# Performance work log

Hardware: AMD Instinct MI355X
Metric: run time of the kernel (lower is better)

The kernel has to match this reference:

```python
import jax, jax.numpy as jnp
import numpy as np


def _ln(x, g, b, eps=1e-5):
    m = x.mean(-1, keepdims=True)
    v = x.var(-1, keepdims=True)
    return (x - m) / jnp.sqrt(v + eps) * g + b


def setup_inputs() -> dict:
    key = jax.random.key(0)
    ks = jax.random.split(key, 10)
    N, H, E, OUT, L = 4096, 256, 131072, 64, 6
    s = 1.0 / np.sqrt(H)
    return {
        "x": jax.random.normal(ks[0], (N, H), jnp.float32),
        "edge_index": jax.random.randint(ks[1], (2, E), 0, N, jnp.int32),
        "sage_wl": jax.random.normal(ks[2], (L, H, H), jnp.float32) * s,   # lin_l (neighbors, has bias)
        "sage_wr": jax.random.normal(ks[3], (L, H, H), jnp.float32) * s,   # lin_r (root, no bias)
        "sage_bl": jnp.zeros((L, H), jnp.float32),
        "ln_g": jnp.ones((L - 1, H), jnp.float32),
        "ln_b": jnp.zeros((L - 1, H), jnp.float32),
        "conv_w": jax.random.normal(ks[4], (3, H, H, 3), jnp.float32) * (1.0 / np.sqrt(3 * H)),  # [layer,O,I,K]
        "conv_b": jnp.zeros((3, H), jnp.float32),
        "cnorm_g": jnp.ones((3, H), jnp.float32),
        "cnorm_b": jnp.zeros((3, H), jnp.float32),
        "in_proj_w": jax.random.normal(ks[5], (6 * H, 2 * H), jnp.float32) * (1.0 / np.sqrt(2 * H)),
        "in_proj_b": jnp.zeros((6 * H,), jnp.float32),
        "out_proj_w": jax.random.normal(ks[6], (2 * H, 2 * H), jnp.float32) * (1.0 / np.sqrt(2 * H)),
        "out_proj_b": jnp.zeros((2 * H,), jnp.float32),
        "anorm_g": jnp.ones((2 * H,), jnp.float32),
        "anorm_b": jnp.zeros((2 * H,), jnp.float32),
        "fuse_w": jax.random.normal(ks[7], (OUT, 2 * H), jnp.float32) * (1.0 / np.sqrt(2 * H)),
        "fuse_b": jnp.zeros((OUT,), jnp.float32),
    }


def reference(x, edge_index, sage_wl, sage_wr, sage_bl, ln_g, ln_b,
              conv_w, conv_b, cnorm_g, cnorm_b,
              in_proj_w, in_proj_b, out_proj_w, out_proj_b,
              anorm_g, anorm_b, fuse_w, fuse_b):
    # Dropout layers act as identity (eval mode).
    N, H = x.shape
    L = sage_wl.shape[0]
    src, dst = edge_index[0], edge_index[1]
    deg = jax.ops.segment_sum(jnp.ones(src.shape[0], x.dtype), dst, num_segments=N)
    deg = jnp.maximum(deg, 1.0)[:, None]
    h = x
    for i in range(L):
        res = h
        # SAGEConv: mean-aggregate neighbor features (gather/scatter), then two linears
        agg = jax.ops.segment_sum(h[src], dst, num_segments=N) / deg
        h = agg @ sage_wl[i].T + sage_bl[i] + h @ sage_wr[i].T
        if i < L - 1:
            h = _ln(h, ln_g[i], ln_b[i])
        h = jax.nn.relu(h) + res  # residual (shapes always match: in==hidden)
    gnn_out = h                                   # [N, H]

    # CNN branch over the node axis: [1, H, N]
    c = gnn_out.T[None]
    for j in range(3):
        c = jax.lax.conv_general_dilated(c, conv_w[j], (1,), ((1, 1),),
                                         dimension_numbers=("NCH", "OIH", "NCH"))
        c = jax.nn.relu(c + conv_b[j][None, :, None])
        c = _ln(c.transpose(0, 2, 1), cnorm_g[j], cnorm_b[j]).transpose(0, 2, 1)
    cnn_out = c[0].T                              # [N, H]

    fused = jnp.concatenate([gnn_out, cnn_out], axis=1)  # [N, 2H]
    E2 = fused.shape[1]
    heads = 4
    hd = E2 // heads
    qkv = fused @ in_proj_w.T + in_proj_b
    q, k, v = jnp.split(qkv, 3, axis=1)
    split_heads = lambda t: t.reshape(N, heads, hd).transpose(1, 0, 2)  # [h, N, hd]
    q, k, v = split_heads(q), split_heads(k), split_heads(v)
    scores = jnp.einsum("hnd,hmd->hnm", q, k) / np.sqrt(hd).astype(np.float32)
    a = jax.nn.softmax(scores, axis=-1)
    o = jnp.einsum("hnm,hmd->hnd", a, v).transpose(1, 0, 2).reshape(N, E2)
    o = o @ out_proj_w.T + out_proj_b
    o = _ln(o, anorm_g, anorm_b)
    return o @ fuse_w.T + fuse_b                  # [N, out_channels]
```

## Files before the change

kernel.cpp:

```cpp
#include <hip/hip_runtime.h>

#define NN 4096
#define HH 256
#define EE 131072

__device__ __constant__ float LN_EPS = 1e-5f;
#define ATT_SCALE 0.08838834764831845f
#define ATT_SHIFT 30.0f

typedef __attribute__((ext_vector_type(8))) short bf16x8_t;
typedef __attribute__((ext_vector_type(4))) float f32x4_t;

__device__ inline ushort f2b(float f) {
  uint u = __float_as_uint(f);
  uint r = (u + 0x7FFF + ((u >> 16) & 1)) >> 16;
  return (ushort)r;
}

__global__ void hist_kernel(const int* __restrict__ ei, int* __restrict__ cnt) {
  int e = blockIdx.x * blockDim.x + threadIdx.x;
  if (e < EE) atomicAdd(&cnt[ei[EE + e]], 1);
}

__global__ __launch_bounds__(1024) void scan_kernel(int* __restrict__ cnt_cursor,
                                                    int* __restrict__ rowptr,
                                                    float* __restrict__ invdeg) {
  __shared__ int part[1024];
  int t = threadIdx.x;
  int base = t * 4;
  int cs[4];
  int s = 0;
  for (int u = 0; u < 4; ++u) { cs[u] = cnt_cursor[base + u]; s += cs[u]; }
  part[t] = s;
  __syncthreads();
  for (int off = 1; off < 1024; off <<= 1) {
    int add = (t >= off) ? part[t - off] : 0;
    int v = part[t];
    __syncthreads();
    part[t] = v + add;
    __syncthreads();
  }
  int excl = (t > 0) ? part[t - 1] : 0;
  for (int u = 0; u < 4; ++u) {
    rowptr[base + u] = excl;
    cnt_cursor[base + u] = excl;
    invdeg[base + u] = 1.0f / (float)max(cs[u], 1);
    excl += cs[u];
  }
  if (t == 1023) rowptr[NN] = excl;
}

__global__ void fill_kernel(const int* __restrict__ ei, int* __restrict__ cursor,
                            int* __restrict__ col) {
  int e = blockIdx.x * blockDim.x + threadIdx.x;
  if (e < EE) {
    int d = ei[EE + e];
    int p = atomicAdd(&cursor[d], 1);
    col[p] = ei[e];
  }
}

__global__ __launch_bounds__(256) void castw(const float* __restrict__ in,
                                             ushort* __restrict__ out) {
  int i4 = (blockIdx.x * 256 + threadIdx.x) * 4;
  float4 v = *(const float4*)(in + i4);
  ushort4 w;
  w.x = f2b(v.x); w.y = f2b(v.y); w.z = f2b(v.z); w.w = f2b(v.w);
  *(ushort4*)(out + i4) = w;
}

__global__ __launch_bounds__(256) void castconv(const float* __restrict__ w,
                                                ushort* __restrict__ o) {
  int idx = blockIdx.x * 256 + threadIdx.x;
  int j = idx / 196608;
  int rem = idx - j * 196608;
  int oc = rem / 768;
  int kk = rem - oc * 768;
  int ks = kk >> 8, ii = kk & 255;
  o[idx] = f2b(w[j * 196608 + oc * 768 + ii * 3 + ks]);
}

__global__ __launch_bounds__(64) void agg_kernel(const float* __restrict__ h,
                                                 const int* __restrict__ rowptr,
                                                 const int* __restrict__ col,
                                                 const float* __restrict__ invdeg,
                                                 ushort* __restrict__ aggb) {
  int n = blockIdx.x;
  int t = threadIdx.x;
  int s = rowptr[n], e = rowptr[n + 1];
  float4 acc = make_float4(0.f, 0.f, 0.f, 0.f);
  for (int j = s; j < e; ++j) {
    int c = col[j];
    const float4 v = *(const float4*)(h + (size_t)c * HH + t * 4);
    acc.x += v.x; acc.y += v.y; acc.z += v.z; acc.w += v.w;
  }
  float id = invdeg[n];
  ushort4 w;
  w.x = f2b(acc.x * id); w.y = f2b(acc.y * id);
  w.z = f2b(acc.z * id); w.w = f2b(acc.w * id);
  *(ushort4*)(aggb + (size_t)n * HH + t * 4) = w;
}

__global__ __launch_bounds__(256) void gemm_mfma(
    const ushort* __restrict__ A0, const ushort* __restrict__ A1,
    const ushort* __restrict__ B0, const ushort* __restrict__ B1,
    const float* __restrict__ bias, float* __restrict__ Cf, ushort* __restrict__ Cb,
    int M, int Nn, int K, int KHA, int KHB, int relu) {
  __shared__ ushort Alds[64][40];
  __shared__ ushort Blds[128][40];
  int t = threadIdx.x;
  int w = t >> 6, l = t & 63, quad = l >> 4, lr = l & 15;
  int wm = w & 1, wn = w >> 1;
  int m0 = blockIdx.x * 64, n0 = blockIdx.y * 128;
  int sr = t >> 2, sc8 = (t & 3) * 8;
  f32x4_t acc[2][4];
#pragma unroll
  for (int s = 0; s < 2; ++s)
#pragma unroll
    for (int q = 0; q < 4; ++q) acc[s][q] = (f32x4_t){0.f, 0.f, 0.f, 0.f};

  for (int k0 = 0; k0 < K; k0 += 32) {
    int kk = k0 + sc8;
    const ushort* ap = (kk < KHA) ? (A0 + (size_t)(m0 + sr) * KHA + kk)
                                  : (A1 + (size_t)(m0 + sr) * (K - KHA) + (kk - KHA));
    uint4 av = *(const uint4*)ap;
    const ushort* bp0 = (kk < KHB) ? (B0 + (size_t)(n0 + sr) * KHB + kk)
                                   : (B1 + (size_t)(n0 + sr) * (K - KHB) + (kk - KHB));
    uint4 bv0 = *(const uint4*)bp0;
    const ushort* bp1 = (kk < KHB) ? (B0 + (size_t)(n0 + 64 + sr) * KHB + kk)
                                   : (B1 + (size_t)(n0 + 64 + sr) * (K - KHB) + (kk - KHB));
    uint4 bv1 = *(const uint4*)bp1;
    __syncthreads();
    *(uint4*)&Alds[sr][sc8] = av;
    *(uint4*)&Blds[sr][sc8] = bv0;
    *(uint4*)&Blds[64 + sr][sc8] = bv1;
    __syncthreads();
    bf16x8_t af[2], bf[4];
#pragma unroll
    for (int s = 0; s < 2; ++s)
      af[s] = *(const bf16x8_t*)&Alds[wm * 32 + s * 16 + lr][quad * 8];
#pragma unroll
    for (int q = 0; q < 4; ++q)
      bf[q] = *(const bf16x8_t*)&Blds[wn * 64 + q * 16 + lr][quad * 8];
#pragma unroll
    for (int s = 0; s < 2; ++s)
#pragma unroll
      for (int q = 0; q < 4; ++q)
        acc[s][q] = __builtin_amdgcn_mfma_f32_16x16x32_bf16(af[s], bf[q], acc[s][q], 0, 0, 0);
  }
#pragma unroll
  for (int s = 0; s < 2; ++s) {
#pragma unroll
    for (int q = 0; q < 4; ++q) {
      int n = n0 + wn * 64 + q * 16 + lr;
      float bb = bias[n];
#pragma unroll
      for (int r = 0; r < 4; ++r) {
        int m = m0 + wm * 32 + s * 16 + quad * 4 + r;
        float v = acc[s][q][r] + bb;
        if (relu) v = fmaxf(v, 0.f);
        if (Cf) Cf[(size_t)m * Nn + n] = v;
        if (Cb) Cb[(size_t)m * Nn + n] = f2b(v);
      }
    }
  }
}

__global__ __launch_bounds__(256) void gemm_dual(
    const ushort* __restrict__ A0, const ushort* __restrict__ B0,
    const float* __restrict__ bias0, float* __restrict__ C0,
    const ushort* __restrict__ A1, const ushort* __restrict__ B1,
    float* __restrict__ C1) {
  __shared__ ushort Alds[64][40];
  __shared__ ushort Blds[128][40];
  int t = threadIdx.x;
  int w = t >> 6, l = t & 63, quad = l >> 4, lr = l & 15;
  int wm = w & 1, wn = w >> 1;
  int m0 = blockIdx.x * 64, n0 = blockIdx.y * 128;
  int z = blockIdx.z;
  const ushort* A = z ? A1 : A0;
  const ushort* B = z ? B1 : B0;
  float* C = z ? C1 : C0;
  int sr = t >> 2, sc8 = (t & 3) * 8;
  f32x4_t acc[2][4];
#pragma unroll
  for (int s = 0; s < 2; ++s)
#pragma unroll
    for (int q = 0; q < 4; ++q) acc[s][q] = (f32x4_t){0.f, 0.f, 0.f, 0.f};

  for (int k0 = 0; k0 < 256; k0 += 32) {
    int kk = k0 + sc8;
    uint4 av = *(const uint4*)(A + (size_t)(m0 + sr) * 256 + kk);
    uint4 bv0 = *(const uint4*)(B + (size_t)(n0 + sr) * 256 + kk);
    uint4 bv1 = *(const uint4*)(B + (size_t)(n0 + 64 + sr) * 256 + kk);
    __syncthreads();
    *(uint4*)&Alds[sr][sc8] = av;
    *(uint4*)&Blds[sr][sc8] = bv0;
    *(uint4*)&Blds[64 + sr][sc8] = bv1;
    __syncthreads();
    bf16x8_t af[2], bf[4];
#pragma unroll
    for (int s = 0; s < 2; ++s)
      af[s] = *(const bf16x8_t*)&Alds[wm * 32 + s * 16 + lr][quad * 8];
#pragma unroll
    for (int q = 0; q < 4; ++q)
      bf[q] = *(const bf16x8_t*)&Blds[wn * 64 + q * 16 + lr][quad * 8];
#pragma unroll
    for (int s = 0; s < 2; ++s)
#pragma unroll
      for (int q = 0; q < 4; ++q)
        acc[s][q] = __builtin_amdgcn_mfma_f32_16x16x32_bf16(af[s], bf[q], acc[s][q], 0, 0, 0);
  }
#pragma unroll
  for (int s = 0; s < 2; ++s) {
#pragma unroll
    for (int q = 0; q < 4; ++q) {
      int n = n0 + wn * 64 + q * 16 + lr;
      float bb = z ? 0.f : bias0[n];
#pragma unroll
      for (int r = 0; r < 4; ++r) {
        int m = m0 + wm * 32 + s * 16 + quad * 4 + r;
        C[(size_t)m * 256 + n] = acc[s][q][r] + bb;
      }
    }
  }
}

__global__ __launch_bounds__(256) void gemm_conv_mfma(
    const ushort* __restrict__ Ab, const ushort* __restrict__ B,
    const float* __restrict__ bias, float* __restrict__ C0, float* __restrict__ C1) {
  __shared__ ushort Alds[64][40];
  __shared__ ushort Blds[128][40];
  int t = threadIdx.x;
  int w = t >> 6, l = t & 63, quad = l >> 4, lr = l & 15;
  int wm = w & 1, wn = w >> 1;
  int m0 = blockIdx.x * 64, n0 = blockIdx.y * 128;
  int z = blockIdx.z;
  float* C = z ? C1 : C0;
  int sr = t >> 2, sc8 = (t & 3) * 8;
  f32x4_t acc[2][4];
#pragma unroll
  for (int s = 0; s < 2; ++s)
#pragma unroll
    for (int q = 0; q < 4; ++q) acc[s][q] = (f32x4_t){0.f, 0.f, 0.f, 0.f};

  for (int k0 = 0; k0 < 384; k0 += 32) {
    int kk = z * 384 + k0 + sc8;
    int ks = kk >> 8, ii = kk & 255;
    int nr = m0 + sr + ks - 1;
    uint4 av = make_uint4(0u, 0u, 0u, 0u);
    if (nr >= 0 && nr < NN) av = *(const uint4*)(Ab + (size_t)nr * HH + ii);
    uint4 bv0 = *(const uint4*)(B + (size_t)(n0 + sr) * 768 + kk);
    uint4 bv1 = *(const uint4*)(B + (size_t)(n0 + 64 + sr) * 768 + kk);
    __syncthreads();
    *(uint4*)&Alds[sr][sc8] = av;
    *(uint4*)&Blds[sr][sc8] = bv0;
    *(uint4*)&Blds[64 + sr][sc8] = bv1;
    __syncthreads();
    bf16x8_t af[2], bf[4];
#pragma unroll
    for (int s = 0; s < 2; ++s)
      af[s] = *(const bf16x8_t*)&Alds[wm * 32 + s * 16 + lr][quad * 8];
#pragma unroll
    for (int q = 0; q < 4; ++q)
      bf[q] = *(const bf16x8_t*)&Blds[wn * 64 + q * 16 + lr][quad * 8];
#pragma unroll
    for (int s = 0; s < 2; ++s)
#pragma unroll
      for (int q = 0; q < 4; ++q)
        acc[s][q] = __builtin_amdgcn_mfma_f32_16x16x32_bf16(af[s], bf[q], acc[s][q], 0, 0, 0);
  }
#pragma unroll
  for (int s = 0; s < 2; ++s) {
#pragma unroll
    for (int q = 0; q < 4; ++q) {
      int n = n0 + wn * 64 + q * 16 + lr;
      float bb = z ? 0.f : bias[n];
#pragma unroll
      for (int r = 0; r < 4; ++r) {
        int m = m0 + wm * 32 + s * 16 + quad * 4 + r;
        C[(size_t)m * HH + n] = acc[s][q][r] + bb;
      }
    }
  }
}

__global__ __launch_bounds__(256) void gemm_std(
    const float* __restrict__ A0, const float* __restrict__ B0,
    const float* __restrict__ bias, float* __restrict__ C,
    int M, int Nn, int K) {
  __shared__ float As[16][68];
  __shared__ float Bs[16][68];
  int t = threadIdx.x;
  int m0 = blockIdx.x * 64, n0 = blockIdx.y * 64;
  int ty = t >> 4, tx = t & 15;
  int lr = t >> 2, lc4 = (t & 3) * 4;
  float acc[4][4] = {};
  for (int k0 = 0; k0 < K; k0 += 16) {
    int kk = k0 + lc4;
    float4 va = *(const float4*)(A0 + (size_t)(m0 + lr) * K + kk);
    As[lc4 + 0][lr] = va.x; As[lc4 + 1][lr] = va.y;
    As[lc4 + 2][lr] = va.z; As[lc4 + 3][lr] = va.w;
    float4 vb = *(const float4*)(B0 + (size_t)(n0 + lr) * K + kk);
    Bs[lc4 + 0][lr] = vb.x; Bs[lc4 + 1][lr] = vb.y;
    Bs[lc4 + 2][lr] = vb.z; Bs[lc4 + 3][lr] = vb.w;
    __syncthreads();
#pragma unroll
    for (int k = 0; k < 16; ++k) {
      float4 a4 = *(const float4*)&As[k][4 * ty];
      float4 b4 = *(const float4*)&Bs[k][4 * tx];
      float av[4] = {a4.x, a4.y, a4.z, a4.w};
      float bv[4] = {b4.x, b4.y, b4.z, b4.w};
#pragma unroll
      for (int i = 0; i < 4; ++i)
#pragma unroll
        for (int j = 0; j < 4; ++j) acc[i][j] += av[i] * bv[j];
    }
    __syncthreads();
  }
#pragma unroll
  for (int i = 0; i < 4; ++i) {
    int m = m0 + 4 * ty + i;
    float o[4];
#pragma unroll
    for (int j = 0; j < 4; ++j) o[j] = acc[i][j] + bias[n0 + 4 * tx + j];
    float4 o4 = make_float4(o[0], o[1], o[2], o[3]);
    *(float4*)(C + (size_t)m * Nn + n0 + 4 * tx) = o4;
  }
}

__global__ __launch_bounds__(256) void ln_fuse(
    const float* __restrict__ x, const float* __restrict__ x2,
    const float* __restrict__ g, const float* __restrict__ b,
    const float* __restrict__ res, float* __restrict__ outf, ushort* __restrict__ outb,
    int D, int do_ln, int relu_res, int prerelu) {
  int row = blockIdx.x, t = threadIdx.x;
  int nv = D >> 8;
  float vals[2];
  float s = 0.f, sq = 0.f;
  for (int u = 0; u < nv; ++u) {
    int c = t + (u << 8);
    float v = x[(size_t)row * D + c];
    if (x2) v += x2[(size_t)row * D + c];
    if (prerelu) v = fmaxf(v, 0.f);
    vals[u] = v; s += v; sq += v * v;
  }
  __shared__ float red[8];
  float m = 0.f, inv = 1.f;
  if (do_ln) {
    for (int off = 32; off >= 1; off >>= 1) {
      s += __shfl_xor(s, off);
      sq += __shfl_xor(sq, off);
    }
    int wid = t >> 6;
    if ((t & 63) == 0) { red[wid] = s; red[4 + wid] = sq; }
    __syncthreads();
    if (t == 0) {
      float S = red[0] + red[1] + red[2] + red[3];
      float Q = red[4] + red[5] + red[6] + red[7];
      float mm = S / D;
      float vv = Q / D - mm * mm;
      red[0] = mm;
      red[1] = rsqrtf(vv + LN_EPS);
    }
    __syncthreads();
    m = red[0]; inv = red[1];
  }
  for (int u = 0; u < nv; ++u) {
    int c = t + (u << 8);
    float y = vals[u];
    if (do_ln) y = (y - m) * inv * g[c] + b[c];
    if (relu_res) y = fmaxf(y, 0.f) + res[(size_t)row * D + c];
    if (outf) outf[(size_t)row * D + c] = y;
    if (outb) outb[(size_t)row * D + c] = f2b(y);
  }
}

__global__ __launch_bounds__(256) void kvpack(const ushort* __restrict__ qkvb,
                                              ushort* __restrict__ Kt,
                                              ushort* __restrict__ VtT) {
  int t = threadIdx.x;
  int n0 = blockIdx.x * 32;
  int by = blockIdx.y;
  int kt = n0 >> 5;
  {
    int head = by >> 2, ks = by & 3;
    int key = t >> 3, e4 = (t & 7) * 4;
    uint2 v = *(const uint2*)(qkvb + (size_t)(n0 + key) * 1536 + 512 + head * 128 + ks * 32 + e4);
    *(uint2*)(Kt + ((((size_t)head * 128 + kt) * 4 + ks) * 32 + key) * 32 + e4) = v;
  }
  __shared__ ushort tile[32][34];
  int d0 = by * 32;
  int tx = t & 31, ty = t >> 5;
#pragma unroll
  for (int u = 0; u < 4; ++u) {
    int r = ty + 8 * u;
    tile[r][tx] = qkvb[(size_t)(n0 + r) * 1536 + 1024 + d0 + tx];
  }
  __syncthreads();
#pragma unroll
  for (int u = 0; u < 4; ++u) {
    int dg = d0 + ty + 8 * u;
    int head = dg >> 7, dl = dg & 127;
    VtT[((((size_t)head * 128 + kt) * 128 + dl) << 5) + tx] = tile[tx][ty + 8 * u];
  }
}

__global__ __launch_bounds__(256, 2) void attn_mfma(const ushort* __restrict__ qkvb,
                                                    const ushort* __restrict__ Kt,
                                                    const ushort* __restrict__ VtT,
                                                    ushort* __restrict__ Ob) {
  __shared__ __align__(16) char smem[66048];
  int t = threadIdx.x;
  int w = t >> 6, l = t & 63;
  int quad = l >> 4, lr = l & 15;
  int head = blockIdx.y;
  int q0 = blockIdx.x * 32;

  ushort* Pl = (ushort*)smem + w * 1280;

  bf16x8_t qf[2][4];
#pragma unroll
  for (int s = 0; s < 2; ++s)
#pragma unroll
    for (int ks = 0; ks < 4; ++ks)
      qf[s][ks] = *(const bf16x8_t*)(qkvb + (size_t)(q0 + s * 16 + lr) * 1536 +
                                     head * 128 + ks * 32 + quad * 8);

  f32x4_t of[2][8];
#pragma unroll
  for (int s = 0; s < 2; ++s)
#pragma unroll
    for (int dt = 0; dt < 8; ++dt) of[s][dt] = (f32x4_t){0.f, 0.f, 0.f, 0.f};
  float den[2][4] = {{0.f, 0.f, 0.f, 0.f}, {0.f, 0.f, 0.f, 0.f}};

  const int lnoff = lr * 32 + quad * 8;
  const int tile0 = w * 32;

  bf16x8_t kfA[4][2];
  {
    const ushort* kb = Kt + (((size_t)head * 128 + tile0) << 12);
#pragma unroll
    for (int ks = 0; ks < 4; ++ks)
#pragma unroll
      for (int ct = 0; ct < 2; ++ct)
        kfA[ks][ct] = *(const bf16x8_t*)(kb + ks * 1024 + ct * 512 + lnoff);
  }

#pragma unroll 2
  for (int tt = 0; tt < 32; ++tt) {
    int kt = tile0 + tt;
    const ushort* vbase = VtT + (((size_t)head * 128 + kt) << 12);

    bf16x8_t vf[8];
#pragma unroll
    for (int dt = 0; dt < 8; ++dt)
      vf[dt] = *(const bf16x8_t*)(vbase + dt * 512 + lnoff);

    bf16x8_t kfB[4][2];
    if (tt < 31) {
      const ushort* kb = Kt + (((size_t)head * 128 + kt + 1) << 12);
#pragma unroll
      for (int ks = 0; ks < 4; ++ks)
#pragma unroll
        for (int ct = 0; ct < 2; ++ct)
          kfB[ks][ct] = *(const bf16x8_t*)(kb + ks * 1024 + ct * 512 + lnoff);
    }

    f32x4_t sf[2][2];
#pragma unroll
    for (int s = 0; s < 2; ++s)
#pragma unroll
      for (int ct = 0; ct < 2; ++ct) sf[s][ct] = (f32x4_t){0.f, 0.f, 0.f, 0.f};
    __builtin_amdgcn_s_setprio(1);
#pragma unroll
    for (int ks = 0; ks < 4; ++ks)
#pragma unroll
      for (int ct = 0; ct < 2; ++ct)
#pragma unroll
        for (int s = 0; s < 2; ++s)
          sf[s][ct] = __builtin_amdgcn_mfma_f32_16x16x32_bf16(qf[s][ks], kfA[ks][ct], sf[s][ct], 0, 0, 0);
    __builtin_amdgcn_s_setprio(0);

#pragma unroll
    for (int s = 0; s < 2; ++s)
#pragma unroll
      for (int ct = 0; ct < 2; ++ct)
#pragma unroll
        for (int r = 0; r < 4; ++r) {
          float e = __expf(sf[s][ct][r] * ATT_SCALE - ATT_SHIFT);
          Pl[(s * 16 + quad * 4 + r) * 40 + ct * 16 + lr] = f2b(e);
          den[s][r] += e;
        }

    __builtin_amdgcn_s_setprio(1);
#pragma unroll
    for (int s = 0; s < 2; ++s) {
      bf16x8_t pf = *(const bf16x8_t*)&Pl[(s * 16 + lr) * 40 + quad * 8];
#pragma unroll
      for (int dt = 0; dt < 8; ++dt)
        of[s][dt] = __builtin_amdgcn_mfma_f32_16x16x32_bf16(pf, vf[dt], of[s][dt], 0, 0, 0);
    }
    __builtin_amdgcn_s_setprio(0);

    if (tt < 31) {
#pragma unroll
      for (int ks = 0; ks < 4; ++ks)
#pragma unroll
        for (int ct = 0; ct < 2; ++ct) kfA[ks][ct] = kfB[ks][ct];
    }
  }

#pragma unroll
  for (int mask = 1; mask < 16; mask <<= 1)
#pragma unroll
    for (int s = 0; s < 2; ++s)
#pragma unroll
      for (int r = 0; r < 4; ++r) den[s][r] += __shfl_xor(den[s][r], mask);

  __syncthreads();
  float* Osum = (float*)smem;
  float* Dsum = (float*)(smem + 65536);
#pragma unroll
  for (int s = 0; s < 2; ++s)
#pragma unroll
    for (int dt = 0; dt < 8; ++dt)
#pragma unroll
      for (int r = 0; r < 4; ++r)
        Osum[w * 4096 + (s * 16 + quad * 4 + r) * 128 + dt * 16 + lr] = of[s][dt][r];
  if (lr == 0) {
#pragma unroll
    for (int s = 0; s < 2; ++s)
#pragma unroll
      for (int r = 0; r < 4; ++r) Dsum[w * 32 + s * 16 + quad * 4 + r] = den[s][r];
  }
  __syncthreads();
#pragma unroll
  for (int e = 0; e < 16; ++e) {
    int idx = l + e * 64;
    int row = w * 8 + (idx >> 7), col = idx & 127;
    float o = Osum[row * 128 + col] + Osum[4096 + row * 128 + col] +
              Osum[8192 + row * 128 + col] + Osum[12288 + row * 128 + col];
    float dn = Dsum[row] + Dsum[32 + row] + Dsum[64 + row] + Dsum[96 + row];
    Ob[(size_t)(q0 + row) * 512 + head * 128 + col] = f2b(o / dn);
  }
}

extern "C" void kernel_launch(void* const* d_in, const int* in_sizes, int n_in,
                              void* d_out, int out_size, void* d_ws, size_t ws_size,
                              hipStream_t stream) {
  const float* x          = (const float*)d_in[0];
  const int*   ei         = (const int*)d_in[1];
  const float* sage_wl    = (const float*)d_in[2];
  const float* sage_wr    = (const float*)d_in[3];
  const float* sage_bl    = (const float*)d_in[4];
  const float* ln_g       = (const float*)d_in[5];
  const float* ln_b       = (const float*)d_in[6];
  const float* conv_w     = (const float*)d_in[7];
  const float* conv_b     = (const float*)d_in[8];
  const float* cnorm_g    = (const float*)d_in[9];
  const float* cnorm_b    = (const float*)d_in[10];
  const float* in_proj_w  = (const float*)d_in[11];
  const float* in_proj_b  = (const float*)d_in[12];
  const float* out_proj_w = (const float*)d_in[13];
  const float* out_proj_b = (const float*)d_in[14];
  const float* anorm_g    = (const float*)d_in[15];
  const float* anorm_b    = (const float*)d_in[16];
  const float* fuse_w     = (const float*)d_in[17];
  const float* fuse_b     = (const float*)d_in[18];
  float* out = (float*)d_out;

  char* ws = (char*)d_ws;
  const size_t MB = 1 << 20;
  int*    rowptr = (int*)(ws + 0);
  int*    cnt    = (int*)(ws + 65536);
  int*    col    = (int*)(ws + 131072);
  float*  invdeg = (float*)(ws + 786432);
  float*  h    = (float*)(ws + 1 * MB);
  ushort* hb   = (ushort*)(ws + 5 * MB);
  ushort* aggb = (ushort*)(ws + 7 * MB);
  float*  tmp  = (float*)(ws + 9 * MB);
  ushort* c0b  = (ushort*)(ws + 13 * MB);
  ushort* c1b  = (ushort*)(ws + 15 * MB);
  ushort* qkvb = (ushort*)(ws + 17 * MB);
  float*  op   = (float*)(ws + 17 * MB);
  float*  tmp2 = (float*)(ws + 25 * MB);
  ushort* Kt   = (ushort*)(ws + 1 * MB);
  ushort* Vt   = (ushort*)(ws + 29 * MB);
  ushort* aob  = (ushort*)(ws + 33 * MB);
  ushort* wlb  = (ushort*)(ws + 37 * MB);
  ushort* wrb  = (ushort*)(ws + 37 * MB + 786432);
  ushort* cvb  = (ushort*)(ws + 37 * MB + 1572864);
  ushort* ipb  = (ushort*)(ws + 37 * MB + 2752512);
  ushort* opb  = (ushort*)(ws + 37 * MB + 4325376);

  castw<<<(6 * 256 * 256) / 1024, 256, 0, stream>>>(sage_wl, wlb);
  castw<<<(6 * 256 * 256) / 1024, 256, 0, stream>>>(sage_wr, wrb);
  castconv<<<(3 * 256 * 768) / 256, 256, 0, stream>>>(conv_w, cvb);
  castw<<<(1536 * 512) / 1024, 256, 0, stream>>>(in_proj_w, ipb);
  castw<<<(512 * 512) / 1024, 256, 0, stream>>>(out_proj_w, opb);

  hipMemsetAsync(cnt, 0, NN * sizeof(int), stream);
  hist_kernel<<<EE / 256, 256, 0, stream>>>(ei, cnt);
  scan_kernel<<<1, 1024, 0, stream>>>(cnt, rowptr, invdeg);
  fill_kernel<<<EE / 256, 256, 0, stream>>>(ei, cnt, col);
  hipMemcpyAsync(h, x, (size_t)NN * HH * sizeof(float), hipMemcpyDeviceToDevice, stream);
  castw<<<(NN * HH) / 1024, 256, 0, stream>>>(x, hb);

  for (int i = 0; i < 6; ++i) {
    agg_kernel<<<NN, 64, 0, stream>>>(h, rowptr, col, invdeg, aggb);
    gemm_dual<<<dim3(64, 2, 2), 256, 0, stream>>>(
        aggb, wlb + (size_t)i * HH * HH, sage_bl + i * HH, tmp,
        hb, wrb + (size_t)i * HH * HH, tmp2);
    int do_ln = (i < 5) ? 1 : 0;
    const float* gp = do_ln ? (ln_g + i * HH) : ln_g;
    const float* bp = do_ln ? (ln_b + i * HH) : ln_b;
    ln_fuse<<<NN, 256, 0, stream>>>(tmp, tmp2, gp, bp, h, h, hb, HH, do_ln, 1, 0);
  }

  const ushort* cin = hb;
  ushort* couts[3] = {c0b, c1b, c0b};
  for (int j = 0; j < 3; ++j) {
    gemm_conv_mfma<<<dim3(64, 2, 2), 256, 0, stream>>>(
        cin, cvb + (size_t)j * HH * 768, conv_b + j * HH, tmp, tmp2);
    ln_fuse<<<NN, 256, 0, stream>>>(tmp, tmp2, cnorm_g + j * HH, cnorm_b + j * HH,
                                    nullptr, nullptr, couts[j], HH, 1, 0, 1);
    cin = couts[j];
  }

  gemm_mfma<<<dim3(64, 12), 256, 0, stream>>>(
      hb, c0b, ipb, nullptr, in_proj_b, nullptr, qkvb, NN, 1536, 512, 256, 1536 * 0 + 512, 0);
  kvpack<<<dim3(NN / 32, 16), 256, 0, stream>>>(qkvb, Kt, Vt);
  attn_mfma<<<dim3(NN / 32, 4), 256, 0, stream>>>(qkvb, Kt, Vt, aob);

  gemm_mfma<<<dim3(64, 4), 256, 0, stream>>>(
      aob, nullptr, opb, nullptr, out_proj_b, op, nullptr, NN, 512, 512, 512, 512, 0);
  ln_fuse<<<NN, 256, 0, stream>>>(op, nullptr, anorm_g, anorm_b, nullptr, op, nullptr, 512, 1, 0, 0);
  gemm_std<<<dim3(64, 1), 256, 0, stream>>>(op, fuse_w, fuse_b, out, NN, 64, 512);
}
```

Baseline: 517.6 us.

## Widen attention blocks to 16 waves and gather SAGE neighbors from bf16

The attention kernel now runs 1024-thread blocks that cover 64 queries. Eight waves split the key tiles for each 32-query half, and partial outputs are reduced through LDS in column chunks with a shared inverse-denominator table. The explicit K-fragment double-buffering is dropped. Separately, neighbor aggregation reads the bf16 copy of h instead of fp32, which halves gather bandwidth but may change rounding. The larger blocks cut the grid to 256 blocks and add more barriers, which could reduce occupancy on a 256-CU device.

```diff
diff --git a/kernel.cpp b/kernel.cpp
--- a/kernel.cpp
+++ b/kernel.cpp
@@ -16,6 +16,7 @@
   uint r = (u + 0x7FFF + ((u >> 16) & 1)) >> 16;
   return (ushort)r;
 }
+__device__ inline float b2f(ushort u) { return __uint_as_float((uint)u << 16); }
 
 __global__ void hist_kernel(const int* __restrict__ ei, int* __restrict__ cnt) {
   int e = blockIdx.x * blockDim.x + threadIdx.x;
@@ -80,7 +81,7 @@
   o[idx] = f2b(w[j * 196608 + oc * 768 + ii * 3 + ks]);
 }
 
-__global__ __launch_bounds__(64) void agg_kernel(const float* __restrict__ h,
+__global__ __launch_bounds__(64) void agg_kernel(const ushort* __restrict__ hb,
                                                  const int* __restrict__ rowptr,
                                                  const int* __restrict__ col,
                                                  const float* __restrict__ invdeg,
@@ -91,8 +92,8 @@
   float4 acc = make_float4(0.f, 0.f, 0.f, 0.f);
   for (int j = s; j < e; ++j) {
     int c = col[j];
-    const float4 v = *(const float4*)(h + (size_t)c * HH + t * 4);
-    acc.x += v.x; acc.y += v.y; acc.z += v.z; acc.w += v.w;
+    ushort4 v = *(const ushort4*)(hb + (size_t)c * HH + t * 4);
+    acc.x += b2f(v.x); acc.y += b2f(v.y); acc.z += b2f(v.z); acc.w += b2f(v.w);
   }
   float id = invdeg[n];
   ushort4 w;
@@ -406,16 +407,17 @@
   }
 }
 
-__global__ __launch_bounds__(256, 2) void attn_mfma(const ushort* __restrict__ qkvb,
-                                                    const ushort* __restrict__ Kt,
-                                                    const ushort* __restrict__ VtT,
-                                                    ushort* __restrict__ Ob) {
-  __shared__ __align__(16) char smem[66048];
+__global__ __launch_bounds__(1024, 4) void attn_mfma(const ushort* __restrict__ qkvb,
+                                                     const ushort* __restrict__ Kt,
+                                                     const ushort* __restrict__ VtT,
+                                                     ushort* __restrict__ Ob) {
+  __shared__ __align__(16) char smem[71936];
   int t = threadIdx.x;
   int w = t >> 6, l = t & 63;
   int quad = l >> 4, lr = l & 15;
+  int qh = w >> 3, ke = w & 7;
   int head = blockIdx.y;
-  int q0 = blockIdx.x * 32;
+  int q0 = blockIdx.x * 64 + qh * 32;
 
   ushort* Pl = (ushort*)smem + w * 1280;
 
@@ -435,38 +437,24 @@
   float den[2][4] = {{0.f, 0.f, 0.f, 0.f}, {0.f, 0.f, 0.f, 0.f}};
 
   const int lnoff = lr * 32 + quad * 8;
-  const int tile0 = w * 32;
-
-  bf16x8_t kfA[4][2];
-  {
-    const ushort* kb = Kt + (((size_t)head * 128 + tile0) << 12);
+  const int tile0 = ke * 16;
+
+  for (int tt = 0; tt < 16; ++tt) {
+    int kt = tile0 + tt;
+    const ushort* kbase = Kt + (((size_t)head * 128 + kt) << 12);
+    const ushort* vbase = VtT + (((size_t)head * 128 + kt) << 12);
+
+    bf16x8_t kf[4][2];
 #pragma unroll
     for (int ks = 0; ks < 4; ++ks)
 #pragma unroll
       for (int ct = 0; ct < 2; ++ct)
-        kfA[ks][ct] = *(const bf16x8_t*)(kb + ks * 1024 + ct * 512 + lnoff);
-  }
-
-#pragma unroll 2
-  for (int tt = 0; tt < 32; ++tt) {
-    int kt = tile0 + tt;
-    const ushort* vbase = VtT + (((size_t)head * 128 + kt) << 12);
-
+        kf[ks][ct] = *(const bf16x8_t*)(kbase + ks * 1024 + ct * 512 + lnoff);
     bf16x8_t vf[8];
 #pragma unroll
     for (int dt = 0; dt < 8; ++dt)
       vf[dt] = *(const bf16x8_t*)(vbase + dt * 512 + lnoff);
 
-    bf16x8_t kfB[4][2];
-    if (tt < 31) {
-      const ushort* kb = Kt + (((size_t)head * 128 + kt + 1) << 12);
-#pragma unroll
-      for (int ks = 0; ks < 4; ++ks)
-#pragma unroll
-        for (int ct = 0; ct < 2; ++ct)
-          kfB[ks][ct] = *(const bf16x8_t*)(kb + ks * 1024 + ct * 512 + lnoff);
-    }
-
     f32x4_t sf[2][2];
 #pragma unroll
     for (int s = 0; s < 2; ++s)
@@ -479,7 +467,7 @@
       for (int ct = 0; ct < 2; ++ct)
 #pragma unroll
         for (int s = 0; s < 2; ++s)
-          sf[s][ct] = __builtin_amdgcn_mfma_f32_16x16x32_bf16(qf[s][ks], kfA[ks][ct], sf[s][ct], 0, 0, 0);
+          sf[s][ct] = __builtin_amdgcn_mfma_f32_16x16x32_bf16(qf[s][ks], kf[ks][ct], sf[s][ct], 0, 0, 0);
     __builtin_amdgcn_s_setprio(0);
 
 #pragma unroll
@@ -502,13 +490,6 @@
         of[s][dt] = __builtin_amdgcn_mfma_f32_16x16x32_bf16(pf, vf[dt], of[s][dt], 0, 0, 0);
     }
     __builtin_amdgcn_s_setprio(0);
-
-    if (tt < 31) {
-#pragma unroll
-      for (int ks = 0; ks < 4; ++ks)
-#pragma unroll
-        for (int ct = 0; ct < 2; ++ct) kfA[ks][ct] = kfB[ks][ct];
-    }
   }
 
 #pragma unroll
@@ -519,15 +500,9 @@
       for (int r = 0; r < 4; ++r) den[s][r] += __shfl_xor(den[s][r], mask);
 
   __syncthreads();
-  float* Osum = (float*)smem;
-  float* Dsum = (float*)(smem + 65536);
-#pragma unroll
-  for (int s = 0; s < 2; ++s)
-#pragma unroll
-    for (int dt = 0; dt < 8; ++dt)
-#pragma unroll
-      for (int r = 0; r < 4; ++r)
-        Osum[w * 4096 + (s * 16 + quad * 4 + r) * 128 + dt * 16 + lr] = of[s][dt][r];
+  float* OS   = (float*)smem;
+  float* Dsum = (float*)(smem + 69632);
+  float* invd = (float*)(smem + 71680);
   if (lr == 0) {
 #pragma unroll
     for (int s = 0; s < 2; ++s)
@@ -535,14 +510,36 @@
       for (int r = 0; r < 4; ++r) Dsum[w * 32 + s * 16 + quad * 4 + r] = den[s][r];
   }
   __syncthreads();
-#pragma unroll
-  for (int e = 0; e < 16; ++e) {
-    int idx = l + e * 64;
-    int row = w * 8 + (idx >> 7), col = idx & 127;
-    float o = Osum[row * 128 + col] + Osum[4096 + row * 128 + col] +
-              Osum[8192 + row * 128 + col] + Osum[12288 + row * 128 + col];
-    float dn = Dsum[row] + Dsum[32 + row] + Dsum[64 + row] + Dsum[96 + row];
-    Ob[(size_t)(q0 + row) * 512 + head * 128 + col] = f2b(o / dn);
+  if (t < 64) {
+    int oh = t >> 5, row = t & 31;
+    float sden = 0.f;
+#pragma unroll
+    for (int j = 0; j < 8; ++j) sden += Dsum[(oh * 8 + j) * 32 + row];
+    invd[t] = 1.0f / sden;
+  }
+  for (int dc = 0; dc < 4; ++dc) {
+#pragma unroll
+    for (int s = 0; s < 2; ++s)
+#pragma unroll
+      for (int u = 0; u < 2; ++u) {
+        int dt = dc * 2 + u;
+#pragma unroll
+        for (int r = 0; r < 4; ++r)
+          OS[w * 1088 + (s * 16 + quad * 4 + r) * 34 + u * 16 + lr] = of[s][dt][r];
+      }
+    __syncthreads();
+#pragma unroll
+    for (int it = 0; it < 2; ++it) {
+      int idx = t + it * 1024;
+      int orow = idx >> 5, c2 = idx & 31;
+      int oh = orow >> 5, row = orow & 31;
+      float sum = 0.f;
+#pragma unroll
+      for (int j = 0; j < 8; ++j) sum += OS[(oh * 8 + j) * 1088 + row * 34 + c2];
+      Ob[(size_t)(blockIdx.x * 64 + orow) * 512 + head * 128 + dc * 32 + c2] =
+          f2b(sum * invd[orow]);
+    }
+    __syncthreads();
   }
 }
 
@@ -608,7 +605,7 @@
   castw<<<(NN * HH) / 1024, 256, 0, stream>>>(x, hb);
 
   for (int i = 0; i < 6; ++i) {
-    agg_kernel<<<NN, 64, 0, stream>>>(h, rowptr, col, invdeg, aggb);
+    agg_kernel<<<NN, 64, 0, stream>>>(hb, rowptr, col, invdeg, aggb);
     gemm_dual<<<dim3(64, 2, 2), 256, 0, stream>>>(
         aggb, wlb + (size_t)i * HH * HH, sage_bl + i * HH, tmp,
         hb, wrb + (size_t)i * HH * HH, tmp2);
@@ -631,7 +628,7 @@
   gemm_mfma<<<dim3(64, 12), 256, 0, stream>>>(
       hb, c0b, ipb, nullptr, in_proj_b, nullptr, qkvb, NN, 1536, 512, 256, 1536 * 0 + 512, 0);
   kvpack<<<dim3(NN / 32, 16), 256, 0, stream>>>(qkvb, Kt, Vt);
-  attn_mfma<<<dim3(NN / 32, 4), 256, 0, stream>>>(qkvb, Kt, Vt, aob);
+  attn_mfma<<<dim3(64, 4), 1024, 0, stream>>>(qkvb, Kt, Vt, aob);
 
   gemm_mfma<<<dim3(64, 4), 256, 0, stream>>>(
       aob, nullptr, opb, nullptr, out_proj_b, op, nullptr, NN, 512, 512, 512, 512, 0);
```

Result: slower. 725.2 us (+40.1%).

## Fuse SAGE and conv GEMMs with LayerNorm epilogues, merge cast kernels

Applied to the files above, without the earlier changes.

The separate SAGE dual-GEMM and conv GEMM kernels plus their LayerNorm/ReLU/residual pass are replaced by single kernels. Each block computes a full 32x256 output row tile with K concatenated, then does bias, LayerNorm, ReLU and the residual in the epilogue, so fp32 intermediates never go through global memory. The five weight-cast kernels are merged into one launch, the memcpy and input cast are fused, and neighbor aggregation now gathers bf16 rows instead of fp32. Trade-offs: only 128 blocks per GEMM, which gives low occupancy on a large GPU, and some precision loss because aggregation reads bf16.

```diff
diff --git a/kernel.cpp b/kernel.cpp
--- a/kernel.cpp
+++ b/kernel.cpp
@@ -16,6 +16,7 @@
   uint r = (u + 0x7FFF + ((u >> 16) & 1)) >> 16;
   return (ushort)r;
 }
+__device__ inline float b2f(ushort u) { return __uint_as_float((uint)u << 16); }
 
 __global__ void hist_kernel(const int* __restrict__ ei, int* __restrict__ cnt) {
   int e = blockIdx.x * blockDim.x + threadIdx.x;
@@ -60,27 +61,64 @@
   }
 }
 
-__global__ __launch_bounds__(256) void castw(const float* __restrict__ in,
-                                             ushort* __restrict__ out) {
+__global__ __launch_bounds__(256) void castall(
+    const float* __restrict__ wl, const float* __restrict__ wr,
+    const float* __restrict__ cw, const float* __restrict__ ip,
+    const float* __restrict__ opw,
+    ushort* __restrict__ wlb, ushort* __restrict__ wrb, ushort* __restrict__ cvb,
+    ushort* __restrict__ ipb, ushort* __restrict__ opb) {
   int i4 = (blockIdx.x * 256 + threadIdx.x) * 4;
-  float4 v = *(const float4*)(in + i4);
+  if (i4 >= 2424832) return;
+  ushort4 o;
+  if (i4 < 393216) {
+    float4 v = *(const float4*)(wl + i4);
+    o.x = f2b(v.x); o.y = f2b(v.y); o.z = f2b(v.z); o.w = f2b(v.w);
+    *(ushort4*)(wlb + i4) = o;
+  } else if (i4 < 786432) {
+    int p = i4 - 393216;
+    float4 v = *(const float4*)(wr + p);
+    o.x = f2b(v.x); o.y = f2b(v.y); o.z = f2b(v.z); o.w = f2b(v.w);
+    *(ushort4*)(wrb + p) = o;
+  } else if (i4 < 1376256) {
+    int p = i4 - 786432;
+    ushort tmp[4];
+#pragma unroll
+    for (int u = 0; u < 4; ++u) {
+      int idx = p + u;
+      int j = idx / 196608;
+      int rem = idx - j * 196608;
+      int oc = rem / 768;
+      int kk = rem - oc * 768;
+      int ks = kk >> 8, ii = kk & 255;
+      tmp[u] = f2b(cw[j * 196608 + oc * 768 + ii * 3 + ks]);
+    }
+    o.x = tmp[0]; o.y = tmp[1]; o.z = tmp[2]; o.w = tmp[3];
+    *(ushort4*)(cvb + p) = o;
+  } else if (i4 < 2162688) {
+    int p = i4 - 1376256;
+    float4 v = *(const float4*)(ip + p);
+    o.x = f2b(v.x); o.y = f2b(v.y); o.z = f2b(v.z); o.w = f2b(v.w);
+    *(ushort4*)(ipb + p) = o;
+  } else {
+    int p = i4 - 2162688;
+    float4 v = *(const float4*)(opw + p);
+    o.x = f2b(v.x); o.y = f2b(v.y); o.z = f2b(v.z); o.w = f2b(v.w);
+    *(ushort4*)(opb + p) = o;
+  }
+}
+
+__global__ __launch_bounds__(256) void copycast(const float* __restrict__ x,
+                                                float* __restrict__ h,
+                                                ushort* __restrict__ hb) {
+  int i4 = (blockIdx.x * 256 + threadIdx.x) * 4;
+  float4 v = *(const float4*)(x + i4);
+  *(float4*)(h + i4) = v;
   ushort4 w;
   w.x = f2b(v.x); w.y = f2b(v.y); w.z = f2b(v.z); w.w = f2b(v.w);
-  *(ushort4*)(out + i4) = w;
-}
-
-__global__ __launch_bounds__(256) void castconv(const float* __restrict__ w,
-                                                ushort* __restrict__ o) {
-  int idx = blockIdx.x * 256 + threadIdx.x;
-  int j = idx / 196608;
-  int rem = idx - j * 196608;
-  int oc = rem / 768;
-  int kk = rem - oc * 768;
-  int ks = kk >> 8, ii = kk & 255;
-  o[idx] = f2b(w[j * 196608 + oc * 768 + ii * 3 + ks]);
-}
-
-__global__ __launch_bounds__(64) void agg_kernel(const float* __restrict__ h,
+  *(ushort4*)(hb + i4) = w;
+}
+
+__global__ __launch_bounds__(64) void agg_kernel(const ushort* __restrict__ hb,
                                                  const int* __restrict__ rowptr,
                                                  const int* __restrict__ col,
                                                  const float* __restrict__ invdeg,
@@ -91,8 +129,8 @@
   float4 acc = make_float4(0.f, 0.f, 0.f, 0.f);
   for (int j = s; j < e; ++j) {
     int c = col[j];
-    const float4 v = *(const float4*)(h + (size_t)c * HH + t * 4);
-    acc.x += v.x; acc.y += v.y; acc.z += v.z; acc.w += v.w;
+    ushort4 v = *(const ushort4*)(hb + (size_t)c * HH + t * 4);
+    acc.x += b2f(v.x); acc.y += b2f(v.y); acc.z += b2f(v.z); acc.w += b2f(v.w);
   }
   float id = invdeg[n];
   ushort4 w;
@@ -166,45 +204,50 @@
   }
 }
 
-__global__ __launch_bounds__(256) void gemm_dual(
-    const ushort* __restrict__ A0, const ushort* __restrict__ B0,
-    const float* __restrict__ bias0, float* __restrict__ C0,
-    const ushort* __restrict__ A1, const ushort* __restrict__ B1,
-    float* __restrict__ C1) {
-  __shared__ ushort Alds[64][40];
-  __shared__ ushort Blds[128][40];
+__global__ __launch_bounds__(256) void sage_fused(
+    const ushort* __restrict__ A0, const ushort* __restrict__ A1,
+    const ushort* __restrict__ B0, const ushort* __restrict__ B1,
+    const float* __restrict__ bias, const float* __restrict__ g,
+    const float* __restrict__ b, float* __restrict__ h, ushort* __restrict__ hb,
+    int do_ln) {
+  __shared__ ushort Alds[32][40];
+  __shared__ ushort Blds[256][40];
   int t = threadIdx.x;
   int w = t >> 6, l = t & 63, quad = l >> 4, lr = l & 15;
-  int wm = w & 1, wn = w >> 1;
-  int m0 = blockIdx.x * 64, n0 = blockIdx.y * 128;
-  int z = blockIdx.z;
-  const ushort* A = z ? A1 : A0;
-  const ushort* B = z ? B1 : B0;
-  float* C = z ? C1 : C0;
-  int sr = t >> 2, sc8 = (t & 3) * 8;
+  int m0 = blockIdx.x * 32;
+  int sr = (t >> 2) & 31, sc8 = (t & 3) * 8;
   f32x4_t acc[2][4];
 #pragma unroll
   for (int s = 0; s < 2; ++s)
 #pragma unroll
     for (int q = 0; q < 4; ++q) acc[s][q] = (f32x4_t){0.f, 0.f, 0.f, 0.f};
 
-  for (int k0 = 0; k0 < 256; k0 += 32) {
-    int kk = k0 + sc8;
-    uint4 av = *(const uint4*)(A + (size_t)(m0 + sr) * 256 + kk);
-    uint4 bv0 = *(const uint4*)(B + (size_t)(n0 + sr) * 256 + kk);
-    uint4 bv1 = *(const uint4*)(B + (size_t)(n0 + 64 + sr) * 256 + kk);
-    __syncthreads();
-    *(uint4*)&Alds[sr][sc8] = av;
-    *(uint4*)&Blds[sr][sc8] = bv0;
-    *(uint4*)&Blds[64 + sr][sc8] = bv1;
+  for (int k0 = 0; k0 < 512; k0 += 32) {
+    uint4 av = make_uint4(0u, 0u, 0u, 0u);
+    if (t < 128) {
+      int kk = k0 + sc8;
+      av = (kk < 256) ? *(const uint4*)(A0 + (size_t)(m0 + sr) * 256 + kk)
+                      : *(const uint4*)(A1 + (size_t)(m0 + sr) * 256 + kk - 256);
+    }
+    uint4 bv[4];
+#pragma unroll
+    for (int c = 0; c < 4; ++c) {
+      int kk = k0 + c * 8;
+      bv[c] = (kk < 256) ? *(const uint4*)(B0 + (size_t)t * 256 + kk)
+                         : *(const uint4*)(B1 + (size_t)t * 256 + kk - 256);
+    }
+    __syncthreads();
+    if (t < 128) *(uint4*)&Alds[sr][sc8] = av;
+#pragma unroll
+    for (int c = 0; c < 4; ++c) *(uint4*)&Blds[t][c * 8] = bv[c];
     __syncthreads();
     bf16x8_t af[2], bf[4];
 #pragma unroll
     for (int s = 0; s < 2; ++s)
-      af[s] = *(const bf16x8_t*)&Alds[wm * 32 + s * 16 + lr][quad * 8];
+      af[s] = *(const bf16x8_t*)&Alds[s * 16 + lr][quad * 8];
 #pragma unroll
     for (int q = 0; q < 4; ++q)
-      bf[q] = *(const bf16x8_t*)&Blds[wn * 64 + q * 16 + lr][quad * 8];
+      bf[q] = *(const bf16x8_t*)&Blds[w * 64 + q * 16 + lr][quad * 8];
 #pragma unroll
     for (int s = 0; s < 2; ++s)
 #pragma unroll
@@ -212,58 +255,121 @@
         acc[s][q] = __builtin_amdgcn_mfma_f32_16x16x32_bf16(af[s], bf[q], acc[s][q], 0, 0, 0);
   }
 #pragma unroll
-  for (int s = 0; s < 2; ++s) {
+  for (int s = 0; s < 2; ++s)
 #pragma unroll
     for (int q = 0; q < 4; ++q) {
-      int n = n0 + wn * 64 + q * 16 + lr;
-      float bb = z ? 0.f : bias0[n];
+      float bb = bias[w * 64 + q * 16 + lr];
+#pragma unroll
+      for (int r = 0; r < 4; ++r) acc[s][q][r] += bb;
+    }
+  float m_[2][4], inv_[2][4];
+  if (do_ln) {
+    float rs[2][4] = {{0.f, 0.f, 0.f, 0.f}, {0.f, 0.f, 0.f, 0.f}};
+    float rq[2][4] = {{0.f, 0.f, 0.f, 0.f}, {0.f, 0.f, 0.f, 0.f}};
+#pragma unroll
+    for (int s = 0; s < 2; ++s)
+#pragma unroll
+      for (int q = 0; q < 4; ++q)
+#pragma unroll
+        for (int r = 0; r < 4; ++r) {
+          float v = acc[s][q][r];
+          rs[s][r] += v; rq[s][r] += v * v;
+        }
+#pragma unroll
+    for (int mask = 1; mask < 16; mask <<= 1)
+#pragma unroll
+      for (int s = 0; s < 2; ++s)
+#pragma unroll
+        for (int r = 0; r < 4; ++r) {
+          rs[s][r] += __shfl_xor(rs[s][r], mask);
+          rq[s][r] += __shfl_xor(rq[s][r], mask);
+        }
+    __syncthreads();
+    float* redS = (float*)&Alds[0][0];
+    float* redQ = redS + 128;
+    if (lr == 0) {
+#pragma unroll
+      for (int s = 0; s < 2; ++s)
+#pragma unroll
+        for (int r = 0; r < 4; ++r) {
+          int row = s * 16 + quad * 4 + r;
+          redS[w * 32 + row] = rs[s][r];
+          redQ[w * 32 + row] = rq[s][r];
+        }
+    }
+    __syncthreads();
+#pragma unroll
+    for (int s = 0; s < 2; ++s)
 #pragma unroll
       for (int r = 0; r < 4; ++r) {
-        int m = m0 + wm * 32 + s * 16 + quad * 4 + r;
-        C[(size_t)m * 256 + n] = acc[s][q][r] + bb;
+        int row = s * 16 + quad * 4 + r;
+        float S = redS[row] + redS[32 + row] + redS[64 + row] + redS[96 + row];
+        float Q = redQ[row] + redQ[32 + row] + redQ[64 + row] + redQ[96 + row];
+        float mm = S * (1.f / 256.f);
+        float vv = Q * (1.f / 256.f) - mm * mm;
+        m_[s][r] = mm;
+        inv_[s][r] = rsqrtf(vv + LN_EPS);
       }
-    }
-  }
-}
-
-__global__ __launch_bounds__(256) void gemm_conv_mfma(
+  }
+#pragma unroll
+  for (int s = 0; s < 2; ++s)
+#pragma unroll
+    for (int q = 0; q < 4; ++q) {
+      int colc = w * 64 + q * 16 + lr;
+      float gg = do_ln ? g[colc] : 0.f;
+      float bb2 = do_ln ? b[colc] : 0.f;
+#pragma unroll
+      for (int r = 0; r < 4; ++r) {
+        int row = m0 + s * 16 + quad * 4 + r;
+        float y = acc[s][q][r];
+        if (do_ln) y = (y - m_[s][r]) * inv_[s][r] * gg + bb2;
+        y = fmaxf(y, 0.f) + h[(size_t)row * 256 + colc];
+        h[(size_t)row * 256 + colc] = y;
+        hb[(size_t)row * 256 + colc] = f2b(y);
+      }
+    }
+}
+
+__global__ __launch_bounds__(256) void conv_fused(
     const ushort* __restrict__ Ab, const ushort* __restrict__ B,
-    const float* __restrict__ bias, float* __restrict__ C0, float* __restrict__ C1) {
-  __shared__ ushort Alds[64][40];
-  __shared__ ushort Blds[128][40];
+    const float* __restrict__ bias, const float* __restrict__ g,
+    const float* __restrict__ b, ushort* __restrict__ outb) {
+  __shared__ ushort Alds[32][40];
+  __shared__ ushort Blds[256][40];
   int t = threadIdx.x;
   int w = t >> 6, l = t & 63, quad = l >> 4, lr = l & 15;
-  int wm = w & 1, wn = w >> 1;
-  int m0 = blockIdx.x * 64, n0 = blockIdx.y * 128;
-  int z = blockIdx.z;
-  float* C = z ? C1 : C0;
-  int sr = t >> 2, sc8 = (t & 3) * 8;
+  int m0 = blockIdx.x * 32;
+  int sr = (t >> 2) & 31, sc8 = (t & 3) * 8;
   f32x4_t acc[2][4];
 #pragma unroll
   for (int s = 0; s < 2; ++s)
 #pragma unroll
     for (int q = 0; q < 4; ++q) acc[s][q] = (f32x4_t){0.f, 0.f, 0.f, 0.f};
 
-  for (int k0 = 0; k0 < 384; k0 += 32) {
-    int kk = z * 384 + k0 + sc8;
-    int ks = kk >> 8, ii = kk & 255;
-    int nr = m0 + sr + ks - 1;
+  for (int k0 = 0; k0 < 768; k0 += 32) {
     uint4 av = make_uint4(0u, 0u, 0u, 0u);
-    if (nr >= 0 && nr < NN) av = *(const uint4*)(Ab + (size_t)nr * HH + ii);
-    uint4 bv0 = *(const uint4*)(B + (size_t)(n0 + sr) * 768 + kk);
-    uint4 bv1 = *(const uint4*)(B + (size_t)(n0 + 64 + sr) * 768 + kk);
-    __syncthreads();
-    *(uint4*)&Alds[sr][sc8] = av;
-    *(uint4*)&Blds[sr][sc8] = bv0;
-    *(uint4*)&Blds[64 + sr][sc8] = bv1;
+    if (t < 128) {
+      int kk = k0 + sc8;
+      int ks = kk >> 8, ii = kk & 255;
+      int nr = m0 + sr + ks - 1;
+      if (nr >= 0 && nr < NN) av = *(const uint4*)(Ab + (size_t)nr * 256 + ii);
+    }
+    uint4 bv[4];
+#pragma unroll
+    for (int c = 0; c < 4; ++c)
+      bv[c] = *(const uint4*)(B + (size_t)t * 768 + k0 + c * 8);
+    __syncthreads();
+    if (t < 128) *(uint4*)&Alds[sr][sc8] = av;
+#pragma unroll
+    for (int c = 0; c < 4; ++c) *(uint4*)&Blds[t][c * 8] = bv[c];
     __syncthreads();
     bf16x8_t af[2], bf[4];
 #pragma unroll
     for (int s = 0; s < 2; ++s)
-      af[s] = *(const bf16x8_t*)&Alds[wm * 32 + s * 16 + lr][quad * 8];
+      af[s] = *(const bf16x8_t*)&Alds[s * 16 + lr][quad * 8];
 #pragma unroll
     for (int q = 0; q < 4; ++q)
-      bf[q] = *(const bf16x8_t*)&Blds[wn * 64 + q * 16 + lr][quad * 8];
+      bf[q] = *(const bf16x8_t*)&Blds[w * 64 + q * 16 + lr][quad * 8];
 #pragma unroll
     for (int s = 0; s < 2; ++s)
 #pragma unroll
@@ -271,18 +377,64 @@
         acc[s][q] = __builtin_amdgcn_mfma_f32_16x16x32_bf16(af[s], bf[q], acc[s][q], 0, 0, 0);
   }
 #pragma unroll
-  for (int s = 0; s < 2; ++s) {
+  for (int s = 0; s < 2; ++s)
 #pragma unroll
     for (int q = 0; q < 4; ++q) {
-      int n = n0 + wn * 64 + q * 16 + lr;
-      float bb = z ? 0.f : bias[n];
+      float bb = bias[w * 64 + q * 16 + lr];
+#pragma unroll
+      for (int r = 0; r < 4; ++r) acc[s][q][r] = fmaxf(acc[s][q][r] + bb, 0.f);
+    }
+  float rs[2][4] = {{0.f, 0.f, 0.f, 0.f}, {0.f, 0.f, 0.f, 0.f}};
+  float rq[2][4] = {{0.f, 0.f, 0.f, 0.f}, {0.f, 0.f, 0.f, 0.f}};
+#pragma unroll
+  for (int s = 0; s < 2; ++s)
+#pragma unroll
+    for (int q = 0; q < 4; ++q)
 #pragma unroll
       for (int r = 0; r < 4; ++r) {
-        int m = m0 + wm * 32 + s * 16 + quad * 4 + r;
-        C[(size_t)m * HH + n] = acc[s][q][r] + bb;
+        float v = acc[s][q][r];
+        rs[s][r] += v; rq[s][r] += v * v;
       }
-    }
-  }
+#pragma unroll
+  for (int mask = 1; mask < 16; mask <<= 1)
+#pragma unroll
+    for (int s = 0; s < 2; ++s)
+#pragma unroll
+      for (int r = 0; r < 4; ++r) {
+        rs[s][r] += __shfl_xor(rs[s][r], mask);
+        rq[s][r] += __shfl_xor(rq[s][r], mask);
+      }
+  __syncthreads();
+  float* redS = (float*)&Alds[0][0];
+  float* redQ = redS + 128;
+  if (lr == 0) {
+#pragma unroll
+    for (int s = 0; s < 2; ++s)
+#pragma unroll
+      for (int r = 0; r < 4; ++r) {
+        int row = s * 16 + quad * 4 + r;
+        redS[w * 32 + row] = rs[s][r];
+        redQ[w * 32 + row] = rq[s][r];
+      }
+  }
+  __syncthreads();
+#pragma unroll
+  for (int s = 0; s < 2; ++s)
+#pragma unroll
+    for (int q = 0; q < 4; ++q) {
+      int colc = w * 64 + q * 16 + lr;
+      float gg = g[colc], bb2 = b[colc];
+#pragma unroll
+      for (int r = 0; r < 4; ++r) {
+        int row = s * 16 + quad * 4 + r;
+        float S = redS[row] + redS[32 + row] + redS[64 + row] + redS[96 + row];
+        float Q = redQ[row] + redQ[32 + row] + redQ[64 + row] + redQ[96 + row];
+        float mm = S * (1.f / 256.f);
+        float vv = Q * (1.f / 256.f) - mm * mm;
+        float y = (acc[s][q][r] - mm) * rsqrtf(vv + LN_EPS) * gg + bb2;
+        outb[(size_t)(m0 + row) * 256 + colc] = f2b(y);
+      }
+    }
 }
 
 __global__ __launch_bounds__(256) void gemm_std(
@@ -330,49 +482,38 @@
 }
 
 __global__ __launch_bounds__(256) void ln_fuse(
-    const float* __restrict__ x, const float* __restrict__ x2,
-    const float* __restrict__ g, const float* __restrict__ b,
-    const float* __restrict__ res, float* __restrict__ outf, ushort* __restrict__ outb,
-    int D, int do_ln, int relu_res, int prerelu) {
+    const float* __restrict__ x, const float* __restrict__ g, const float* __restrict__ b,
+    float* __restrict__ outf, int D) {
   int row = blockIdx.x, t = threadIdx.x;
   int nv = D >> 8;
   float vals[2];
   float s = 0.f, sq = 0.f;
   for (int u = 0; u < nv; ++u) {
-    int c = t + (u << 8);
-    float v = x[(size_t)row * D + c];
-    if (x2) v += x2[(size_t)row * D + c];
-    if (prerelu) v = fmaxf(v, 0.f);
+    float v = x[(size_t)row * D + t + (u << 8)];
     vals[u] = v; s += v; sq += v * v;
   }
   __shared__ float red[8];
-  float m = 0.f, inv = 1.f;
-  if (do_ln) {
-    for (int off = 32; off >= 1; off >>= 1) {
-      s += __shfl_xor(s, off);
-      sq += __shfl_xor(sq, off);
-    }
-    int wid = t >> 6;
-    if ((t & 63) == 0) { red[wid] = s; red[4 + wid] = sq; }
-    __syncthreads();
-    if (t == 0) {
-      float S = red[0] + red[1] + red[2] + red[3];
-      float Q = red[4] + red[5] + red[6] + red[7];
-      float mm = S / D;
-      float vv = Q / D - mm * mm;
-      red[0] = mm;
-      red[1] = rsqrtf(vv + LN_EPS);
-    }
-    __syncthreads();
-    m = red[0]; inv = red[1];
-  }
+  for (int off = 32; off >= 1; off >>= 1) {
+    s += __shfl_xor(s, off);
+    sq += __shfl_xor(sq, off);
+  }
+  int wid = t >> 6;
+  if ((t & 63) == 0) { red[wid] = s; red[4 + wid] = sq; }
+  __syncthreads();
+  if (t == 0) {
+    float S = red[0] + red[1] + red[2] + red[3];
+    float Q = red[4] + red[5] + red[6] + red[7];
+    float mm = S / D;
+    float vv = Q / D - mm * mm;
+    red[0] = mm;
+    red[1] = rsqrtf(vv + LN_EPS);
+  }
+  __syncthreads();
+  float m = red[0], inv = red[1];
   for (int u = 0; u < nv; ++u) {
     int c = t + (u << 8);
-    float y = vals[u];
-    if (do_ln) y = (y - m) * inv * g[c] + b[c];
-    if (relu_res) y = fmaxf(y, 0.f) + res[(size_t)row * D + c];
-    if (outf) outf[(size_t)row * D + c] = y;
-    if (outb) outb[(size_t)row * D + c] = f2b(y);
+    float y = (vals[u] - m) * inv * g[c] + b[c];
+    outf[(size_t)row * D + c] = y;
   }
 }
 
@@ -579,12 +720,10 @@
   float*  h    = (float*)(ws + 1 * MB);
   ushort* hb   = (ushort*)(ws + 5 * MB);
   ushort* aggb = (ushort*)(ws + 7 * MB);
-  float*  tmp  = (float*)(ws + 9 * MB);
   ushort* c0b  = (ushort*)(ws + 13 * MB);
   ushort* c1b  = (ushort*)(ws + 15 * MB);
   ushort* qkvb = (ushort*)(ws + 17 * MB);
   float*  op   = (float*)(ws + 17 * MB);
-  float*  tmp2 = (float*)(ws + 25 * MB);
   ushort* Kt   = (ushort*)(ws + 1 * MB);
   ushort* Vt   = (ushort*)(ws + 29 * MB);
   ushort* aob  = (ushort*)(ws + 33 * MB);
@@ -594,47 +733,41 @@
   ushort* ipb  = (ushort*)(ws + 37 * MB + 2752512);
   ushort* opb  = (ushort*)(ws + 37 * MB + 4325376);
 
-  castw<<<(6 * 256 * 256) / 1024, 256, 0, stream>>>(sage_wl, wlb);
-  castw<<<(6 * 256 * 256) / 1024, 256, 0, stream>>>(sage_wr, wrb);
-  castconv<<<(3 * 256 * 768) / 256, 256, 0, stream>>>(conv_w, cvb);
-  castw<<<(1536 * 512) / 1024, 256, 0, stream>>>(in_proj_w, ipb);
-  castw<<<(512 * 512) / 1024, 256, 0, stream>>>(out_proj_w, opb);
+  castall<<<2368, 256, 0, stream>>>(sage_wl, sage_wr, conv_w, in_proj_w, out_proj_w,
+                                    wlb, wrb, cvb, ipb, opb);
 
   hipMemsetAsync(cnt, 0, NN * sizeof(int), stream);
   hist_kernel<<<EE / 256, 256, 0, stream>>>(ei, cnt);
   scan_kernel<<<1, 1024, 0, stream>>>(cnt, rowptr, invdeg);
   fill_kernel<<<EE / 256, 256, 0, stream>>>(ei, cnt, col);
-  hipMemcpyAsync(h, x, (size_t)NN * HH * sizeof(float), hipMemcpyDeviceToDevice, stream);
-  castw<<<(NN * HH) / 1024, 256, 0, stream>>>(x, hb);
+  copycast<<<(NN * HH) / 1024, 256, 0, stream>>>(x, h, hb);
 
   for (int i = 0; i < 6; ++i) {
-    agg_kernel<<<NN, 64, 0, stream>>>(h, rowptr, col, invdeg, aggb);
-    gemm_dual<<<dim3(64, 2, 2), 256, 0, stream>>>(
-        aggb, wlb + (size_t)i * HH * HH, sage_bl + i * HH, tmp,
-        hb, wrb + (size_t)i * HH * HH, tmp2);
+    agg_kernel<<<NN, 64, 0, stream>>>(hb, rowptr, col, invdeg, aggb);
     int do_ln = (i < 5) ? 1 : 0;
     const float* gp = do_ln ? (ln_g + i * HH) : ln_g;
     const float* bp = do_ln ? (ln_b + i * HH) : ln_b;
-    ln_fuse<<<NN, 256, 0, stream>>>(tmp, tmp2, gp, bp, h, h, hb, HH, do_ln, 1, 0);
+    sage_fused<<<128, 256, 0, stream>>>(
+        aggb, hb, wlb + (size_t)i * HH * HH, wrb + (size_t)i * HH * HH,
+        sage_bl + i * HH, gp, bp, h, hb, do_ln);
   }
 
   const ushort* cin = hb;
   ushort* couts[3] = {c0b, c1b, c0b};
   for (int j = 0; j < 3; ++j) {
-    gemm_conv_mfma<<<dim3(64, 2, 2), 256, 0, stream>>>(
-        cin, cvb + (size_t)j * HH * 768, conv_b + j * HH, tmp, tmp2);
-    ln_fuse<<<NN, 256, 0, stream>>>(tmp, tmp2, cnorm_g + j * HH, cnorm_b + j * HH,
-                                    nullptr, nullptr, couts[j], HH, 1, 0, 1);
+    conv_fused<<<128, 256, 0, stream>>>(
+        cin, cvb + (size_t)j * HH * 768, conv_b + j * HH,
+        cnorm_g + j * HH, cnorm_b + j * HH, couts[j]);
     cin = couts[j];
   }
 
   gemm_mfma<<<dim3(64, 12), 256, 0, stream>>>(
-      hb, c0b, ipb, nullptr, in_proj_b, nullptr, qkvb, NN, 1536, 512, 256, 1536 * 0 + 512, 0);
+      hb, c0b, ipb, nullptr, in_proj_b, nullptr, qkvb, NN, 1536, 512, 256, 512, 0);
   kvpack<<<dim3(NN / 32, 16), 256, 0, stream>>>(qkvb, Kt, Vt);
   attn_mfma<<<dim3(NN / 32, 4), 256, 0, stream>>>(qkvb, Kt, Vt, aob);
 
   gemm_mfma<<<dim3(64, 4), 256, 0, stream>>>(
       aob, nullptr, opb, nullptr, out_proj_b, op, nullptr, NN, 512, 512, 512, 512, 0);
-  ln_fuse<<<NN, 256, 0, stream>>>(op, nullptr, anorm_g, anorm_b, nullptr, op, nullptr, 512, 1, 0, 0);
+  ln_fuse<<<NN, 256, 0, stream>>>(op, anorm_g, anorm_b, op, 512);
   gemm_std<<<dim3(64, 1), 256, 0, stream>>>(op, fuse_w, fuse_b, out, NN, 64, 512);
 }
```

Result: slower. 692.8 us (+33.9%).
